# Kernel tuning notes

Measured on AMD Instinct MI355X. Metric: run time of the kernel, lower is better.

The kernel has to match this reference:

```python
import jax, jax.numpy as jnp
import numpy as np

DIM = 512
NUM_HEADS = 8
B, NW, W = 8, 64, 64  # batch, num_windows, window_size


def setup_inputs() -> dict:
    key = jax.random.key(0)
    k1, k2, k3 = jax.random.split(key, 3)
    x = jax.random.normal(k1, (B, NW, W, DIM), dtype=jnp.float32)
    w_qkv = jax.random.normal(k2, (DIM, 3 * DIM), dtype=jnp.float32) * (DIM ** -0.5)
    w_proj = jax.random.normal(k3, (DIM, DIM), dtype=jnp.float32) * (DIM ** -0.5)
    b_proj = jnp.zeros((DIM,), dtype=jnp.float32)
    return {"x": x, "w_qkv": w_qkv, "w_proj": w_proj, "b_proj": b_proj}


def reference(x, w_qkv, w_proj, b_proj):
    batch, nw, w, dim = x.shape
    heads = NUM_HEADS
    dh = dim // heads
    scale = dh ** -0.5
    # qkv projection (no bias): [B, nW, W, 3*dim]
    qkv = jnp.einsum('bnwc,cd->bnwd', x, w_qkv)
    # -> [B, nW, W, 3, H, dh] -> [3, B, H, nW, W, dh]
    qkv = qkv.reshape(batch, nw, w, 3, heads, dh)
    qkv = jnp.transpose(qkv, (3, 0, 4, 1, 2, 5))
    q, k, v = qkv[0], qkv[1], qkv[2]
    # attention logits per window: [B, H, nW, W, W]
    attn = jnp.einsum('bhnqd,bhnkd->bhnqk', q, k) * scale
    attn = jax.nn.softmax(attn, axis=-1)
    # [B, H, nW, W, dh]
    out = jnp.einsum('bhnqk,bhnkd->bhnqd', attn, v)
    # faithful raw reshape (no transpose), matching the TF source
    out = out.reshape(batch, nw, w, dim)
    return jnp.einsum('bnwc,cd->bnwd', out, w_proj) + b_proj
```

## Files before the change

### kernel.cpp

```cpp
#include <hip/hip_runtime.h>
#include <hip/hip_bf16.h>

typedef __bf16 bf16_t;
typedef __bf16 bf16x8 __attribute__((ext_vector_type(8)));
typedef float f32x4 __attribute__((ext_vector_type(4)));

__global__ __launch_bounds__(256) void transpose_cast_kernel(
    const float* __restrict__ src, bf16_t* __restrict__ dst, int R, int C)
{
    __shared__ float tile[32][33];
    const int bx = blockIdx.x;
    const int by = blockIdx.y;
    const int t  = threadIdx.x;
    const int i0 = t >> 5;
    const int j  = t & 31;
#pragma unroll
    for (int p = 0; p < 4; ++p) {
        int i = i0 + p * 8;
        tile[i][j] = src[(long)(by * 32 + i) * C + bx * 32 + j];
    }
    __syncthreads();
#pragma unroll
    for (int p = 0; p < 4; ++p) {
        int i = i0 + p * 8;
        dst[(long)(bx * 32 + i) * R + by * 32 + j] = (bf16_t)tile[j][i];
    }
}

__global__ __launch_bounds__(256) void qkv_attn_kernel(
    const float*  __restrict__ x,
    const bf16_t* __restrict__ wT,
    bf16_t* __restrict__ ao)
{
    __shared__ bf16_t arena1[64 * 72];
    __shared__ bf16_t arena2[192 * 72];
    __shared__ bf16_t lVT[64 * 72];

    bf16_t* const lXc = arena1;
    bf16_t* const lP  = arena1;
    bf16_t* const lW  = arena2;
    bf16_t* const lQ  = arena2;
    bf16_t* const lK  = arena2 + 64 * 72;

    const int wid = blockIdx.x;
    const int bb  = wid >> 6;
    const int nw  = wid & 63;
    const float* xw = x + (long)wid * 64 * 512;

    const int t    = threadIdx.x;
    const int wave = t >> 6;
    const int lane = t & 63;
    const int lr   = lane & 15;
    const int q    = lane >> 4;

    const float scale = 0.125f;

    for (int h = 0; h < 8; ++h) {
        f32x4 acc[12];
#pragma unroll
        for (int j = 0; j < 12; ++j) acc[j] = (f32x4)0.0f;

        for (int kc = 0; kc < 8; ++kc) {
            const int k0 = kc * 64;
#pragma unroll
            for (int p = 0; p < 2; ++p) {
                const int v = t + p * 256;
                const int r = v >> 3, c = (v & 7) * 8;
                const float* rp = xw + (long)r * 512 + k0 + c;
                f32x4 f0 = *(const f32x4*)rp;
                f32x4 f1 = *(const f32x4*)(rp + 4);
                bf16x8 o;
                o[0] = (bf16_t)f0[0]; o[1] = (bf16_t)f0[1];
                o[2] = (bf16_t)f0[2]; o[3] = (bf16_t)f0[3];
                o[4] = (bf16_t)f1[0]; o[5] = (bf16_t)f1[1];
                o[6] = (bf16_t)f1[2]; o[7] = (bf16_t)f1[3];
                *(bf16x8*)&lXc[r * 72 + c] = o;
            }
#pragma unroll
            for (int p = 0; p < 6; ++p) {
                const int v = t + p * 256;
                const int nr = v >> 3, c = (v & 7) * 8;
                const int g = nr >> 6, i = nr & 63;
                *(bf16x8*)&lW[nr * 72 + c] =
                    *(const bf16x8*)(wT + (long)(g * 512 + h * 64 + i) * 512 + k0 + c);
            }
            __syncthreads();
#pragma unroll
            for (int ks = 0; ks < 64; ks += 32) {
                bf16x8 af = *(const bf16x8*)&lXc[(wave * 16 + lr) * 72 + ks + q * 8];
#pragma unroll
                for (int j = 0; j < 12; ++j) {
                    bf16x8 bf = *(const bf16x8*)&lW[(j * 16 + lr) * 72 + ks + q * 8];
                    acc[j] = __builtin_amdgcn_mfma_f32_16x16x32_bf16(af, bf, acc[j], 0, 0, 0);
                }
            }
            __syncthreads();
        }

#pragma unroll
        for (int j = 0; j < 4; ++j)
#pragma unroll
            for (int reg = 0; reg < 4; ++reg) {
                const int row = wave * 16 + q * 4 + reg;
                lQ[row * 72 + j * 16 + lr] = (bf16_t)acc[j][reg];
            }
#pragma unroll
        for (int j = 4; j < 8; ++j)
#pragma unroll
            for (int reg = 0; reg < 4; ++reg) {
                const int row = wave * 16 + q * 4 + reg;
                lK[row * 72 + (j - 4) * 16 + lr] = (bf16_t)acc[j][reg];
            }
#pragma unroll
        for (int j = 8; j < 12; ++j)
#pragma unroll
            for (int reg = 0; reg < 4; ++reg) {
                const int row = wave * 16 + q * 4 + reg;
                lVT[((j - 8) * 16 + lr) * 72 + row] = (bf16_t)acc[j][reg];
            }
        __syncthreads();

        f32x4 s[4];
#pragma unroll
        for (int j = 0; j < 4; ++j) s[j] = (f32x4)0.0f;
#pragma unroll
        for (int ks = 0; ks < 64; ks += 32) {
            bf16x8 aq = *(const bf16x8*)&lQ[(wave * 16 + lr) * 72 + ks + q * 8];
#pragma unroll
            for (int j = 0; j < 4; ++j) {
                bf16x8 bk = *(const bf16x8*)&lK[(j * 16 + lr) * 72 + ks + q * 8];
                s[j] = __builtin_amdgcn_mfma_f32_16x16x32_bf16(aq, bk, s[j], 0, 0, 0);
            }
        }

#pragma unroll
        for (int reg = 0; reg < 4; ++reg) {
            float m = fmaxf(fmaxf(s[0][reg], s[1][reg]), fmaxf(s[2][reg], s[3][reg]));
#pragma unroll
            for (int d = 1; d < 16; d <<= 1) m = fmaxf(m, __shfl_xor(m, d));
            float p[4];
            float sum = 0.0f;
#pragma unroll
            for (int j = 0; j < 4; ++j) {
                p[j] = __expf((s[j][reg] - m) * scale);
                sum += p[j];
            }
#pragma unroll
            for (int d = 1; d < 16; d <<= 1) sum += __shfl_xor(sum, d);
            const float inv = 1.0f / sum;
            const int row = wave * 16 + q * 4 + reg;
#pragma unroll
            for (int j = 0; j < 4; ++j)
                lP[row * 72 + j * 16 + lr] = (bf16_t)(p[j] * inv);
        }

        f32x4 o[4];
#pragma unroll
        for (int d4 = 0; d4 < 4; ++d4) o[d4] = (f32x4)0.0f;
#pragma unroll
        for (int ks = 0; ks < 64; ks += 32) {
            bf16x8 ap = *(const bf16x8*)&lP[(wave * 16 + lr) * 72 + ks + q * 8];
#pragma unroll
            for (int d4 = 0; d4 < 4; ++d4) {
                bf16x8 bv = *(const bf16x8*)&lVT[(d4 * 16 + lr) * 72 + ks + q * 8];
                o[d4] = __builtin_amdgcn_mfma_f32_16x16x32_bf16(ap, bv, o[d4], 0, 0, 0);
            }
        }

        bf16_t* aop = ao + ((long)bb * 4096 + (long)h * 512 + nw * 8) * 512;
#pragma unroll
        for (int d4 = 0; d4 < 4; ++d4)
#pragma unroll
            for (int reg = 0; reg < 4; ++reg) {
                const int wr = wave * 16 + q * 4 + reg;
                aop[(long)(wr >> 3) * 512 + (wr & 7) * 64 + d4 * 16 + lr] =
                    (bf16_t)o[d4][reg];
            }
        __syncthreads();
    }
}

#define LDP 72

__global__ __launch_bounds__(256) void gemm2_kernel(
    const bf16_t* __restrict__ A,
    const bf16_t* __restrict__ Bt,
    const float*  __restrict__ bias,
    float* __restrict__ C,
    int M, int N, int K)
{
    __shared__ bf16_t lA[128 * LDP];
    __shared__ bf16_t lB[128 * LDP];

    const int tid  = threadIdx.x;
    const int wave = tid >> 6;
    const int lane = tid & 63;
    const int wm   = wave >> 1;
    const int wn   = wave & 1;
    const int lr   = lane & 15;
    const int q    = lane >> 4;

    const long arow0 = (long)blockIdx.y * 128;
    const long brow0 = (long)blockIdx.x * 128;

    f32x4 acc[4][4];
#pragma unroll
    for (int i = 0; i < 4; ++i)
#pragma unroll
        for (int j = 0; j < 4; ++j) acc[i][j] = (f32x4)0.0f;

    const int srow = tid >> 3;
    const int scol = (tid & 7) * 8;

    const int nk = K / 64;
    for (int kt = 0; kt < nk; ++kt) {
        const bf16_t* Ag = A + arow0 * K + kt * 64;
        const bf16_t* Bg = Bt + brow0 * K + kt * 64;
        bf16x8 av[4], bv[4];
#pragma unroll
        for (int p = 0; p < 4; ++p) {
            const int r = srow + p * 32;
            av[p] = *(const bf16x8*)(Ag + (long)r * K + scol);
            bv[p] = *(const bf16x8*)(Bg + (long)r * K + scol);
        }
#pragma unroll
        for (int p = 0; p < 4; ++p) {
            const int r = srow + p * 32;
            *(bf16x8*)&lA[r * LDP + scol] = av[p];
            *(bf16x8*)&lB[r * LDP + scol] = bv[p];
        }
        __syncthreads();
#pragma unroll
        for (int ks = 0; ks < 64; ks += 32) {
            bf16x8 af[4], bf[4];
#pragma unroll
            for (int i = 0; i < 4; ++i)
                af[i] = *(const bf16x8*)&lA[(wm * 64 + i * 16 + lr) * LDP + ks + q * 8];
#pragma unroll
            for (int j = 0; j < 4; ++j)
                bf[j] = *(const bf16x8*)&lB[(wn * 64 + j * 16 + lr) * LDP + ks + q * 8];
#pragma unroll
            for (int i = 0; i < 4; ++i)
#pragma unroll
                for (int j = 0; j < 4; ++j)
                    acc[i][j] = __builtin_amdgcn_mfma_f32_16x16x32_bf16(
                        af[i], bf[j], acc[i][j], 0, 0, 0);
        }
        __syncthreads();
    }

#pragma unroll
    for (int i = 0; i < 4; ++i) {
        const long r = arow0 + wm * 64 + i * 16 + q * 4;
#pragma unroll
        for (int j = 0; j < 4; ++j) {
            const long c = brow0 + wn * 64 + j * 16 + lr;
            const float bv2 = bias[c];
#pragma unroll
            for (int reg = 0; reg < 4; ++reg) {
                C[(r + reg) * N + c] = acc[i][j][reg] + bv2;
            }
        }
    }
}

extern "C" void kernel_launch(void* const* d_in, const int* in_sizes, int n_in,
                              void* d_out, int out_size, void* d_ws, size_t ws_size,
                              hipStream_t stream)
{
    (void)in_sizes; (void)n_in; (void)out_size; (void)ws_size;
    const float* x     = (const float*)d_in[0];
    const float* wqkv  = (const float*)d_in[1];
    const float* wproj = (const float*)d_in[2];
    const float* bproj = (const float*)d_in[3];
    float* out = (float*)d_out;

    bf16_t* wT = (bf16_t*)d_ws;
    bf16_t* pT = wT + (size_t)1536 * 512;
    bf16_t* ao = pT + (size_t)512 * 512;

    transpose_cast_kernel<<<dim3(48, 16), 256, 0, stream>>>(wqkv, wT, 512, 1536);
    transpose_cast_kernel<<<dim3(16, 16), 256, 0, stream>>>(wproj, pT, 512, 512);

    qkv_attn_kernel<<<512, 256, 0, stream>>>(x, wT, ao);

    gemm2_kernel<<<dim3(4, 256), 256, 0, stream>>>(
        ao, pT, bproj, out, 32768, 512, 512);
}
```

Before: 254.7 us.

## Split attention kernel per head across blocks and add XCD-aware block remapping

The fused QKV+attention kernel previously looped over all 8 heads inside one block per window, giving only 512 blocks. Each head now gets its own block (4096 blocks), which raises occupancy and parallelism. In exchange, the x window tile is re-read from global memory once per head instead of once per window. Block indices are remapped so that all heads of a window, and neighbouring row tiles in the projection GEMM, land on the same XCD to share L2. lVT is folded into the W arena to reduce LDS use.

After: 228.9 us. 1.11x faster.

```diff
diff --git a/kernel.cpp b/kernel.cpp
--- a/kernel.cpp
+++ b/kernel.cpp
@@ -34,15 +34,20 @@
 {
     __shared__ bf16_t arena1[64 * 72];
     __shared__ bf16_t arena2[192 * 72];
-    __shared__ bf16_t lVT[64 * 72];
 
     bf16_t* const lXc = arena1;
     bf16_t* const lP  = arena1;
     bf16_t* const lW  = arena2;
     bf16_t* const lQ  = arena2;
     bf16_t* const lK  = arena2 + 64 * 72;
-
-    const int wid = blockIdx.x;
+    bf16_t* const lVT = arena2 + 128 * 72;
+
+    const int id  = blockIdx.x;
+    const int xcd = id & 7;
+    const int s   = id >> 3;
+    const int wid = xcd * 64 + (s >> 3);
+    const int h   = s & 7;
+
     const int bb  = wid >> 6;
     const int nw  = wid & 63;
     const float* xw = x + (long)wid * 64 * 512;
@@ -55,129 +60,127 @@
 
     const float scale = 0.125f;
 
-    for (int h = 0; h < 8; ++h) {
-        f32x4 acc[12];
-#pragma unroll
-        for (int j = 0; j < 12; ++j) acc[j] = (f32x4)0.0f;
-
-        for (int kc = 0; kc < 8; ++kc) {
-            const int k0 = kc * 64;
-#pragma unroll
-            for (int p = 0; p < 2; ++p) {
-                const int v = t + p * 256;
-                const int r = v >> 3, c = (v & 7) * 8;
-                const float* rp = xw + (long)r * 512 + k0 + c;
-                f32x4 f0 = *(const f32x4*)rp;
-                f32x4 f1 = *(const f32x4*)(rp + 4);
-                bf16x8 o;
-                o[0] = (bf16_t)f0[0]; o[1] = (bf16_t)f0[1];
-                o[2] = (bf16_t)f0[2]; o[3] = (bf16_t)f0[3];
-                o[4] = (bf16_t)f1[0]; o[5] = (bf16_t)f1[1];
-                o[6] = (bf16_t)f1[2]; o[7] = (bf16_t)f1[3];
-                *(bf16x8*)&lXc[r * 72 + c] = o;
+    f32x4 acc[12];
+#pragma unroll
+    for (int j = 0; j < 12; ++j) acc[j] = (f32x4)0.0f;
+
+    for (int kc = 0; kc < 8; ++kc) {
+        const int k0 = kc * 64;
+#pragma unroll
+        for (int p = 0; p < 2; ++p) {
+            const int v = t + p * 256;
+            const int r = v >> 3, c = (v & 7) * 8;
+            const float* rp = xw + (long)r * 512 + k0 + c;
+            f32x4 f0 = *(const f32x4*)rp;
+            f32x4 f1 = *(const f32x4*)(rp + 4);
+            bf16x8 o;
+            o[0] = (bf16_t)f0[0]; o[1] = (bf16_t)f0[1];
+            o[2] = (bf16_t)f0[2]; o[3] = (bf16_t)f0[3];
+            o[4] = (bf16_t)f1[0]; o[5] = (bf16_t)f1[1];
+            o[6] = (bf16_t)f1[2]; o[7] = (bf16_t)f1[3];
+            *(bf16x8*)&lXc[r * 72 + c] = o;
+        }
+#pragma unroll
+        for (int p = 0; p < 6; ++p) {
+            const int v = t + p * 256;
+            const int nr = v >> 3, c = (v & 7) * 8;
+            const int g = nr >> 6, i = nr & 63;
+            *(bf16x8*)&lW[nr * 72 + c] =
+                *(const bf16x8*)(wT + (long)(g * 512 + h * 64 + i) * 512 + k0 + c);
+        }
+        __syncthreads();
+#pragma unroll
+        for (int ks = 0; ks < 64; ks += 32) {
+            bf16x8 af = *(const bf16x8*)&lXc[(wave * 16 + lr) * 72 + ks + q * 8];
+#pragma unroll
+            for (int j = 0; j < 12; ++j) {
+                bf16x8 bf = *(const bf16x8*)&lW[(j * 16 + lr) * 72 + ks + q * 8];
+                acc[j] = __builtin_amdgcn_mfma_f32_16x16x32_bf16(af, bf, acc[j], 0, 0, 0);
             }
-#pragma unroll
-            for (int p = 0; p < 6; ++p) {
-                const int v = t + p * 256;
-                const int nr = v >> 3, c = (v & 7) * 8;
-                const int g = nr >> 6, i = nr & 63;
-                *(bf16x8*)&lW[nr * 72 + c] =
-                    *(const bf16x8*)(wT + (long)(g * 512 + h * 64 + i) * 512 + k0 + c);
-            }
-            __syncthreads();
-#pragma unroll
-            for (int ks = 0; ks < 64; ks += 32) {
-                bf16x8 af = *(const bf16x8*)&lXc[(wave * 16 + lr) * 72 + ks + q * 8];
-#pragma unroll
-                for (int j = 0; j < 12; ++j) {
-                    bf16x8 bf = *(const bf16x8*)&lW[(j * 16 + lr) * 72 + ks + q * 8];
-                    acc[j] = __builtin_amdgcn_mfma_f32_16x16x32_bf16(af, bf, acc[j], 0, 0, 0);
-                }
-            }
-            __syncthreads();
-        }
-
+        }
+        __syncthreads();
+    }
+
+#pragma unroll
+    for (int j = 0; j < 4; ++j)
+#pragma unroll
+        for (int reg = 0; reg < 4; ++reg) {
+            const int row = wave * 16 + q * 4 + reg;
+            lQ[row * 72 + j * 16 + lr] = (bf16_t)acc[j][reg];
+        }
+#pragma unroll
+    for (int j = 4; j < 8; ++j)
+#pragma unroll
+        for (int reg = 0; reg < 4; ++reg) {
+            const int row = wave * 16 + q * 4 + reg;
+            lK[row * 72 + (j - 4) * 16 + lr] = (bf16_t)acc[j][reg];
+        }
+#pragma unroll
+    for (int j = 8; j < 12; ++j)
+#pragma unroll
+        for (int reg = 0; reg < 4; ++reg) {
+            const int row = wave * 16 + q * 4 + reg;
+            lVT[((j - 8) * 16 + lr) * 72 + row] = (bf16_t)acc[j][reg];
+        }
+    __syncthreads();
+
+    f32x4 sAcc[4];
+#pragma unroll
+    for (int j = 0; j < 4; ++j) sAcc[j] = (f32x4)0.0f;
+#pragma unroll
+    for (int ks = 0; ks < 64; ks += 32) {
+        bf16x8 aq = *(const bf16x8*)&lQ[(wave * 16 + lr) * 72 + ks + q * 8];
+#pragma unroll
+        for (int j = 0; j < 4; ++j) {
+            bf16x8 bk = *(const bf16x8*)&lK[(j * 16 + lr) * 72 + ks + q * 8];
+            sAcc[j] = __builtin_amdgcn_mfma_f32_16x16x32_bf16(aq, bk, sAcc[j], 0, 0, 0);
+        }
+    }
+
+#pragma unroll
+    for (int reg = 0; reg < 4; ++reg) {
+        float m = fmaxf(fmaxf(sAcc[0][reg], sAcc[1][reg]),
+                        fmaxf(sAcc[2][reg], sAcc[3][reg]));
+#pragma unroll
+        for (int d = 1; d < 16; d <<= 1) m = fmaxf(m, __shfl_xor(m, d));
+        float p[4];
+        float sum = 0.0f;
+#pragma unroll
+        for (int j = 0; j < 4; ++j) {
+            p[j] = __expf((sAcc[j][reg] - m) * scale);
+            sum += p[j];
+        }
+#pragma unroll
+        for (int d = 1; d < 16; d <<= 1) sum += __shfl_xor(sum, d);
+        const float inv = 1.0f / sum;
+        const int row = wave * 16 + q * 4 + reg;
 #pragma unroll
         for (int j = 0; j < 4; ++j)
-#pragma unroll
-            for (int reg = 0; reg < 4; ++reg) {
-                const int row = wave * 16 + q * 4 + reg;
-                lQ[row * 72 + j * 16 + lr] = (bf16_t)acc[j][reg];
-            }
-#pragma unroll
-        for (int j = 4; j < 8; ++j)
-#pragma unroll
-            for (int reg = 0; reg < 4; ++reg) {
-                const int row = wave * 16 + q * 4 + reg;
-                lK[row * 72 + (j - 4) * 16 + lr] = (bf16_t)acc[j][reg];
-            }
-#pragma unroll
-        for (int j = 8; j < 12; ++j)
-#pragma unroll
-            for (int reg = 0; reg < 4; ++reg) {
-                const int row = wave * 16 + q * 4 + reg;
-                lVT[((j - 8) * 16 + lr) * 72 + row] = (bf16_t)acc[j][reg];
-            }
-        __syncthreads();
-
-        f32x4 s[4];
-#pragma unroll
-        for (int j = 0; j < 4; ++j) s[j] = (f32x4)0.0f;
-#pragma unroll
-        for (int ks = 0; ks < 64; ks += 32) {
-            bf16x8 aq = *(const bf16x8*)&lQ[(wave * 16 + lr) * 72 + ks + q * 8];
-#pragma unroll
-            for (int j = 0; j < 4; ++j) {
-                bf16x8 bk = *(const bf16x8*)&lK[(j * 16 + lr) * 72 + ks + q * 8];
-                s[j] = __builtin_amdgcn_mfma_f32_16x16x32_bf16(aq, bk, s[j], 0, 0, 0);
-            }
-        }
-
-#pragma unroll
-        for (int reg = 0; reg < 4; ++reg) {
-            float m = fmaxf(fmaxf(s[0][reg], s[1][reg]), fmaxf(s[2][reg], s[3][reg]));
-#pragma unroll
-            for (int d = 1; d < 16; d <<= 1) m = fmaxf(m, __shfl_xor(m, d));
-            float p[4];
-            float sum = 0.0f;
-#pragma unroll
-            for (int j = 0; j < 4; ++j) {
-                p[j] = __expf((s[j][reg] - m) * scale);
-                sum += p[j];
-            }
-#pragma unroll
-            for (int d = 1; d < 16; d <<= 1) sum += __shfl_xor(sum, d);
-            const float inv = 1.0f / sum;
-            const int row = wave * 16 + q * 4 + reg;
-#pragma unroll
-            for (int j = 0; j < 4; ++j)
-                lP[row * 72 + j * 16 + lr] = (bf16_t)(p[j] * inv);
-        }
-
-        f32x4 o[4];
-#pragma unroll
-        for (int d4 = 0; d4 < 4; ++d4) o[d4] = (f32x4)0.0f;
-#pragma unroll
-        for (int ks = 0; ks < 64; ks += 32) {
-            bf16x8 ap = *(const bf16x8*)&lP[(wave * 16 + lr) * 72 + ks + q * 8];
-#pragma unroll
-            for (int d4 = 0; d4 < 4; ++d4) {
-                bf16x8 bv = *(const bf16x8*)&lVT[(d4 * 16 + lr) * 72 + ks + q * 8];
-                o[d4] = __builtin_amdgcn_mfma_f32_16x16x32_bf16(ap, bv, o[d4], 0, 0, 0);
-            }
-        }
-
-        bf16_t* aop = ao + ((long)bb * 4096 + (long)h * 512 + nw * 8) * 512;
-#pragma unroll
-        for (int d4 = 0; d4 < 4; ++d4)
-#pragma unroll
-            for (int reg = 0; reg < 4; ++reg) {
-                const int wr = wave * 16 + q * 4 + reg;
-                aop[(long)(wr >> 3) * 512 + (wr & 7) * 64 + d4 * 16 + lr] =
-                    (bf16_t)o[d4][reg];
-            }
-        __syncthreads();
-    }
+            lP[row * 72 + j * 16 + lr] = (bf16_t)(p[j] * inv);
+    }
+
+    f32x4 o[4];
+#pragma unroll
+    for (int d4 = 0; d4 < 4; ++d4) o[d4] = (f32x4)0.0f;
+#pragma unroll
+    for (int ks = 0; ks < 64; ks += 32) {
+        bf16x8 ap = *(const bf16x8*)&lP[(wave * 16 + lr) * 72 + ks + q * 8];
+#pragma unroll
+        for (int d4 = 0; d4 < 4; ++d4) {
+            bf16x8 bv = *(const bf16x8*)&lVT[(d4 * 16 + lr) * 72 + ks + q * 8];
+            o[d4] = __builtin_amdgcn_mfma_f32_16x16x32_bf16(ap, bv, o[d4], 0, 0, 0);
+        }
+    }
+
+    bf16_t* aop = ao + ((long)bb * 4096 + (long)h * 512 + nw * 8) * 512;
+#pragma unroll
+    for (int d4 = 0; d4 < 4; ++d4)
+#pragma unroll
+        for (int reg = 0; reg < 4; ++reg) {
+            const int wr = wave * 16 + q * 4 + reg;
+            aop[(long)(wr >> 3) * 512 + (wr & 7) * 64 + d4 * 16 + lr] =
+                (bf16_t)o[d4][reg];
+        }
 }
 
 #define LDP 72
@@ -200,8 +203,14 @@
     const int lr   = lane & 15;
     const int q    = lane >> 4;
 
-    const long arow0 = (long)blockIdx.y * 128;
-    const long brow0 = (long)blockIdx.x * 128;
+    const int id  = blockIdx.x;
+    const int xcd = id & 7;
+    const int s   = id >> 3;
+    const int bm  = xcd * 32 + (s >> 2);
+    const int bn  = s & 3;
+
+    const long arow0 = (long)bm * 128;
+    const long brow0 = (long)bn * 128;
 
     f32x4 acc[4][4];
 #pragma unroll
@@ -282,8 +291,8 @@
     transpose_cast_kernel<<<dim3(48, 16), 256, 0, stream>>>(wqkv, wT, 512, 1536);
     transpose_cast_kernel<<<dim3(16, 16), 256, 0, stream>>>(wproj, pT, 512, 512);
 
-    qkv_attn_kernel<<<512, 256, 0, stream>>>(x, wT, ao);
-
-    gemm2_kernel<<<dim3(4, 256), 256, 0, stream>>>(
+    qkv_attn_kernel<<<4096, 256, 0, stream>>>(x, wT, ao);
+
+    gemm2_kernel<<<1024, 256, 0, stream>>>(
         ao, pT, bproj, out, 32768, 512, 512);
 }
```
